# Kernel tuning notes

Hardware: AMD Instinct MI355X
Metric: run time of the kernel (lower is better)

The kernel has to match this reference:

```python
import jax, jax.numpy as jnp
import numpy as np

B, T, HID = 1, 2048, 2048
H = 16            # num_heads == num_key_value_heads
D = HID // H      # head_dim == feature_dim == 128
EPS = 1e-5


def _layer_norm(x, eps=1e-5):
    mu = jnp.mean(x, axis=-1, keepdims=True)
    var = jnp.mean((x - mu) ** 2, axis=-1, keepdims=True)
    return (x - mu) * jax.lax.rsqrt(var + eps)


def _feature_map(x, gamma, beta):
    # ReBased feature map, flatten=False (parallel mode): affine then LayerNorm
    return _layer_norm(x * gamma + beta)


def setup_inputs() -> dict:
    key = jax.random.key(0)
    ks = jax.random.split(key, 8)
    s = HID ** -0.5
    return {
        "hidden_states": jax.random.normal(ks[0], (B, T, HID), jnp.float32),
        "Wq": jax.random.normal(ks[1], (HID, HID), jnp.float32) * s,
        "Wk": jax.random.normal(ks[2], (HID, HID), jnp.float32) * s,
        "Wv": jax.random.normal(ks[3], (HID, HID), jnp.float32) * s,
        "Wo": jax.random.normal(ks[4], (HID, HID), jnp.float32) * s,
        "gamma": 1.0 + 0.1 * jax.random.normal(ks[5], (D,), jnp.float32),
        "beta": 0.1 * jax.random.normal(ks[6], (D,), jnp.float32),
    }


def reference(hidden_states, Wq, Wk, Wv, Wo, gamma, beta):
    b, t, _ = hidden_states.shape
    # projections (nn.Linear: x @ W.T), split into heads: [b, t, h, d]
    q = (hidden_states @ Wq.T).reshape(b, t, H, D)
    k = (hidden_states @ Wk.T).reshape(b, t, H, D)
    v = (hidden_states @ Wv.T).reshape(b, t, H, D)
    # ReBased feature map (no quadratic flatten in parallel mode)
    q = _feature_map(q, gamma, beta)
    k = _feature_map(k, gamma, beta)
    # parallel_rebased: scale q, quadratic score, causal mask, normalize
    q = q * (D ** -0.5)
    attn = jnp.einsum('bqhd,bkhd->bhqk', q, k) ** 2  # (q.k)^2
    mask = jnp.tril(jnp.ones((t, t), dtype=bool))
    attn = jnp.where(mask, attn, 0.0)
    o = jnp.einsum('bhqk,bkhd->bqhd', attn, v)       # [b, t, h, d]
    z = jnp.sum(attn, axis=-1)                       # [b, h, t]
    o = o / (jnp.swapaxes(z, 1, 2)[..., None] + EPS)
    o = o.reshape(b, t, H * D)
    return o @ Wo.T
```

## Files before the change

kernel.cpp:

```cpp
#include <hip/hip_runtime.h>
#include <hip/hip_bf16.h>
#include <stdint.h>

typedef __bf16 bf16;
typedef __bf16 v8bf __attribute__((ext_vector_type(8)));
typedef float  v4f  __attribute__((ext_vector_type(4)));

#define TSEQ   2048
#define HIDDIM 2048
#define NHEAD  16
#define HDIM   128

__device__ __forceinline__ void async16(void* lds, const void* g)
{
    __builtin_amdgcn_global_load_lds(
        (__attribute__((address_space(1))) void*)(uintptr_t)g,
        (__attribute__((address_space(3))) void*)(unsigned int)(uintptr_t)lds,
        16, 0, 0);
}

__global__ __launch_bounds__(256) void conv5(const float* __restrict__ s0, bf16* __restrict__ d0,
                                             const float* __restrict__ s1, bf16* __restrict__ d1,
                                             const float* __restrict__ s2, bf16* __restrict__ d2,
                                             const float* __restrict__ s3, bf16* __restrict__ d3,
                                             const float* __restrict__ s4, bf16* __restrict__ d4)
{
    const float* src; bf16* dst;
    switch (blockIdx.y) {
        case 0: src = s0; dst = d0; break;
        case 1: src = s1; dst = d1; break;
        case 2: src = s2; dst = d2; break;
        case 3: src = s3; dst = d3; break;
        default: src = s4; dst = d4; break;
    }
    const size_t i = ((size_t)blockIdx.x * 256 + threadIdx.x) * 8;
    const float4 a = *(const float4*)(src + i);
    const float4 b = *(const float4*)(src + i + 4);
    v8bf o;
    o[0] = (bf16)a.x; o[1] = (bf16)a.y; o[2] = (bf16)a.z; o[3] = (bf16)a.w;
    o[4] = (bf16)b.x; o[5] = (bf16)b.y; o[6] = (bf16)b.z; o[7] = (bf16)b.w;
    *(v8bf*)(dst + i) = o;
}


#define PBAR() do { __builtin_amdgcn_sched_barrier(0); __builtin_amdgcn_s_barrier(); \
                    __builtin_amdgcn_sched_barrier(0); } while (0)

#define ST(shalf, ghalf) do { \
    async16((shalf) + w*512,        (ghalf) + (size_t)(srow0)*2048); \
    async16((shalf) + 4096 + w*512, (ghalf) + (size_t)(srow0 + 64)*2048); \
} while (0)

#define RD_A(buf, mh) do { _Pragma("unroll") \
    for (int mi_ = 0; mi_ < 4; ++mi_) { \
        const bf16* p_ = &sA[(buf)*16384 + (wm*128 + (mh)*64 + mi_*16 + lr)*64]; \
        a[mi_][0] = *(const v8bf*)(p_ + c0); \
        a[mi_][1] = *(const v8bf*)(p_ + c1); } } while (0)

#define RD_B(buf, nh) do { _Pragma("unroll") \
    for (int nj_ = 0; nj_ < 2; ++nj_) { \
        const bf16* p_ = &sB[(buf)*16384 + (wn*64 + (nh)*32 + nj_*16 + lr)*64]; \
        b[(nh)*2+nj_][0] = *(const v8bf*)(p_ + c0); \
        b[(nh)*2+nj_][1] = *(const v8bf*)(p_ + c1); } } while (0)

#define MQ(mh, nh) do { _Pragma("unroll") \
    for (int mi_ = 0; mi_ < 4; ++mi_) { _Pragma("unroll") \
        for (int nj_ = 0; nj_ < 2; ++nj_) { \
            acc[(mh)*4+mi_][(nh)*2+nj_] = __builtin_amdgcn_mfma_f32_16x16x32_bf16( \
                a[mi_][0], b[(nh)*2+nj_][0], acc[(mh)*4+mi_][(nh)*2+nj_], 0, 0, 0); \
            acc[(mh)*4+mi_][(nh)*2+nj_] = __builtin_amdgcn_mfma_f32_16x16x32_bf16( \
                a[mi_][1], b[(nh)*2+nj_][1], acc[(mh)*4+mi_][(nh)*2+nj_], 0, 0, 0); \
        } } } while (0)

__global__ __launch_bounds__(512, 2) void gemm_qkv8(const bf16* __restrict__ A,
    const bf16* __restrict__ Wq, const bf16* __restrict__ Wk, const bf16* __restrict__ Wv,
    bf16* __restrict__ qb, bf16* __restrict__ kb, bf16* __restrict__ vb)
{
    __shared__ __attribute__((aligned(16))) bf16 sA[2*16384];
    __shared__ __attribute__((aligned(16))) bf16 sB[2*16384];
    const int which = blockIdx.x >> 3;
    const int n0 = (blockIdx.x & 7) * 256;
    const int m0 = blockIdx.y * 256;
    const bf16* B = (which == 0) ? Wq : (which == 1) ? Wk : Wv;
    bf16* C = (which == 0) ? qb : (which == 1) ? kb : vb;

    const int tid  = threadIdx.x, l = tid & 63, w = tid >> 6;
    const int wm   = w >> 2, wn = w & 3;
    const int quad = l >> 4, lr = l & 15;
    const int srow0 = w*8 + (l>>3);
    const int scol  = ((l & 7) ^ ((l >> 3) & 7)) * 8;
    const int c0 = (( quad     ) ^ (lr & 7)) * 8;
    const int c1 = ((quad + 4  ) ^ (lr & 7)) * 8;

    const bf16* Ag = A + (size_t)m0 * 2048 + scol;
    const bf16* Bg = B + (size_t)n0 * 2048 + scol;

    v4f  acc[8][4] = {};
    v8bf a[4][2], b[4][2];

    ST(&sA[0],          Ag);
    ST(&sA[8192],       Ag + (size_t)128*2048);
    ST(&sB[0],          Bg);
    ST(&sB[8192],       Bg + (size_t)128*2048);
    ST(&sB[16384],      Bg + 64);
    ST(&sB[16384+8192], Bg + (size_t)128*2048 + 64);
    asm volatile("s_waitcnt vmcnt(4)" ::: "memory");
    __builtin_amdgcn_s_barrier();
    __builtin_amdgcn_sched_barrier(0);

#pragma unroll 1
    for (int it = 0; it < 16; ++it) {
        const int k1 = it*128 + 64;
        const int k2 = (it*128 + 128) & 2047;
        const int k3 = (it*128 + 192) & 2047;

        RD_A(0, 0); RD_B(0, 0);
        ST(&sA[16384], Ag + k1);
        PBAR(); __builtin_amdgcn_s_setprio(1); MQ(0, 0); __builtin_amdgcn_s_setprio(0); PBAR();
        RD_B(0, 1);
        ST(&sA[16384+8192], Ag + (size_t)128*2048 + k1);
        PBAR(); __builtin_amdgcn_s_setprio(1); MQ(0, 1); __builtin_amdgcn_s_setprio(0); PBAR();
        RD_A(0, 1);
        ST(&sB[0], Bg + k2);
        PBAR(); __builtin_amdgcn_s_setprio(1); MQ(1, 0); __builtin_amdgcn_s_setprio(0); PBAR();
        ST(&sB[8192], Bg + (size_t)128*2048 + k2);
        asm volatile("s_waitcnt vmcnt(4)" ::: "memory");
        PBAR(); __builtin_amdgcn_s_setprio(1); MQ(1, 1); __builtin_amdgcn_s_setprio(0); PBAR();
        RD_A(1, 0); RD_B(1, 0);
        ST(&sA[0], Ag + k2);
        PBAR(); __builtin_amdgcn_s_setprio(1); MQ(0, 0); __builtin_amdgcn_s_setprio(0); PBAR();
        RD_B(1, 1);
        ST(&sA[8192], Ag + (size_t)128*2048 + k2);
        PBAR(); __builtin_amdgcn_s_setprio(1); MQ(0, 1); __builtin_amdgcn_s_setprio(0); PBAR();
        RD_A(1, 1);
        ST(&sB[16384], Bg + k3);
        PBAR(); __builtin_amdgcn_s_setprio(1); MQ(1, 0); __builtin_amdgcn_s_setprio(0); PBAR();
        ST(&sB[16384+8192], Bg + (size_t)128*2048 + k3);
        asm volatile("s_waitcnt vmcnt(4)" ::: "memory");
        PBAR(); __builtin_amdgcn_s_setprio(1); MQ(1, 1); __builtin_amdgcn_s_setprio(0); PBAR();
    }

#pragma unroll
    for (int mi = 0; mi < 8; ++mi) {
        const int row = m0 + wm*128 + (mi >> 2)*64 + (mi & 3)*16 + quad*4;
#pragma unroll
        for (int nj = 0; nj < 4; ++nj) {
            const int col = n0 + wn*64 + (nj >> 1)*32 + (nj & 1)*16 + lr;
#pragma unroll
            for (int r = 0; r < 4; ++r)
                C[(size_t)(row + r)*2048 + col] = (bf16)acc[mi][nj][r];
        }
    }
}

__global__ __launch_bounds__(256) void gemm_out(const bf16* __restrict__ A,
    const bf16* __restrict__ B, float* __restrict__ C)
{
    __shared__ __attribute__((aligned(16))) bf16 sA[128*32];
    __shared__ __attribute__((aligned(16))) bf16 sB[64*32];
    const int m0 = blockIdx.y * 128, n0 = blockIdx.x * 64;
    const int K = HIDDIM, ldc = HIDDIM;
    const int tid  = threadIdx.x;
    const int lane = tid & 63;
    const int w    = tid >> 6;
    const int wm   = w >> 1, wn = w & 1;
    const int quad = lane >> 4, lr = lane & 15;
    const int srow = lane >> 2;
    const int scol = (lane & 3) * 8;

    const bf16* gA0 = A + (size_t)(m0 + w*32 + srow) * K + scol;
    const bf16* gB0 = B + (size_t)(n0 + w*16 + srow) * K + scol;
    bf16* lA0 = &sA[w*1024];
    bf16* lB0 = &sB[w*512];

    v4f acc[4][2] = {};

    for (int kt = 0; kt < K; kt += 32) {
        __syncthreads();
        async16(lA0,       gA0 + kt);
        async16(lA0 + 512, gA0 + (size_t)16*K + kt);
        async16(lB0,       gB0 + kt);
        __syncthreads();
        v8bf a[4], b[2];
#pragma unroll
        for (int i = 0; i < 4; ++i)
            a[i] = *(const v8bf*)&sA[(wm*64 + i*16 + lr)*32 + quad*8];
#pragma unroll
        for (int j = 0; j < 2; ++j)
            b[j] = *(const v8bf*)&sB[(wn*32 + j*16 + lr)*32 + quad*8];
#pragma unroll
        for (int i = 0; i < 4; ++i)
#pragma unroll
            for (int j = 0; j < 2; ++j)
                acc[i][j] = __builtin_amdgcn_mfma_f32_16x16x32_bf16(a[i], b[j], acc[i][j], 0, 0, 0);
    }

#pragma unroll
    for (int i = 0; i < 4; ++i) {
        const int row_b = m0 + wm*64 + i*16 + quad*4;
#pragma unroll
        for (int j = 0; j < 2; ++j) {
            const int col = n0 + wn*32 + j*16 + lr;
#pragma unroll
            for (int r = 0; r < 4; ++r)
                C[(size_t)(row_b + r)*ldc + col] = acc[i][j][r];
        }
    }
}

__global__ __launch_bounds__(256) void fmap(bf16* __restrict__ qb, bf16* __restrict__ kb,
                                            const float* __restrict__ gamma,
                                            const float* __restrict__ beta)
{
    const int rid  = blockIdx.x * 4 + (threadIdx.x >> 6);
    const int lane = threadIdx.x & 63;
    bf16* base = (rid < TSEQ*NHEAD) ? (qb + (size_t)rid * HDIM)
                                    : (kb + (size_t)(rid - TSEQ*NHEAD) * HDIM);
    const float scale = (rid < TSEQ*NHEAD) ? 0.08838834764831845f : 1.0f;

    const bf16 x0b = base[lane*2], x1b = base[lane*2+1];
    const float g0 = gamma[lane*2], g1 = gamma[lane*2+1];
    const float b0 = beta[lane*2],  b1 = beta[lane*2+1];
    float x0 = (float)x0b*g0 + b0;
    float x1 = (float)x1b*g1 + b1;
    float s  = x0 + x1;
    float sq = x0*x0 + x1*x1;
#pragma unroll
    for (int off = 1; off < 64; off <<= 1) { s += __shfl_xor(s, off); sq += __shfl_xor(sq, off); }
    const float mu   = s * (1.0f/128.0f);
    float var        = sq * (1.0f/128.0f) - mu*mu;
    var = fmaxf(var, 0.0f);
    const float rstd = rsqrtf(var + 1e-5f);
    base[lane*2]   = (bf16)((x0 - mu) * rstd * scale);
    base[lane*2+1] = (bf16)((x1 - mu) * rstd * scale);
}

__global__ __launch_bounds__(256) void transpose2048(const bf16* __restrict__ src,
                                                     bf16* __restrict__ dst)
{
    __shared__ __attribute__((aligned(16))) bf16 tile[64][72];
    const int t0 = blockIdx.y * 64, c0 = blockIdx.x * 64;
    const int tid = threadIdx.x;
    const int r = tid >> 3;
    const int c = (tid & 7) * 8;
#pragma unroll
    for (int p = 0; p < 2; ++p) {
        const int rr = r + p*32;
        *(v8bf*)&tile[rr][c] = *(const v8bf*)(src + (size_t)(t0+rr)*HIDDIM + c0 + c);
    }
    __syncthreads();
#pragma unroll
    for (int p = 0; p < 2; ++p) {
        const int orow = r + p*32;
        v8bf o;
#pragma unroll
        for (int i = 0; i < 8; ++i) o[i] = tile[c + i][orow];
        *(v8bf*)(dst + (size_t)(c0+orow)*HIDDIM + t0 + c) = o;
    }
}

__global__ __launch_bounds__(512, 2) void attn(const bf16* __restrict__ qb,
                                               const bf16* __restrict__ kb,
                                               const bf16* __restrict__ vt,
                                               bf16* __restrict__ ob)
{
    __shared__ __attribute__((aligned(16))) bf16 sK[2*64*136];
    __shared__ __attribute__((aligned(16))) bf16 sV[2*128*72];
    __shared__ __attribute__((aligned(16))) bf16 sS[2*64*72];
    __shared__ __attribute__((aligned(16))) float sO[64*129];
    __shared__ __attribute__((aligned(16))) float sZ[64*17];

    const int h    = blockIdx.y;
    const int pr   = blockIdx.x;
    const int tid  = threadIdx.x, lane = tid & 63;
    const int w    = tid >> 6;
    const int g    = w >> 2;
    const int ww   = w & 3;
    const int quad = lane >> 4, lr = lane & 15;
    const int rs   = tid >> 4;
    const int cs   = (tid & 15) * 8;

#pragma unroll
    for (int ti = 0; ti < 2; ++ti) {
        const int tile = ti ? pr : (31 - pr);
        const int nch  = tile + 1;

        v8bf qa[4];
        {
            const bf16* q0 = qb + (size_t)(tile*64 + ww*16 + lr)*HIDDIM + h*HDIM + quad*8;
#pragma unroll
            for (int ks = 0; ks < 4; ++ks)
                qa[ks] = *(const v8bf*)(q0 + ks*32);
        }

        v4f  o[8] = {};
        float z[4] = {0.f, 0.f, 0.f, 0.f};

        v8bf curK[4], curV[4], nxtK[4], nxtV[4];
#pragma unroll
        for (int p = 0; p < 4; ++p) {
            curK[p] = *(const v8bf*)(kb + (size_t)(rs + p*32)*HIDDIM + h*HDIM + cs);
            curV[p] = *(const v8bf*)(vt + (size_t)(h*HDIM + rs + p*32)*HIDDIM + cs);
        }

        for (int ich = 0; ich < nch; ich += 2) {
            __syncthreads();
#pragma unroll
            for (int p = 0; p < 4; ++p) {
                const int r = rs + p*32;
                *(v8bf*)&sK[(r>>6)*8704 + (r&63)*136 + cs] = curK[p];
            }
#pragma unroll
            for (int p = 0; p < 4; ++p)
                *(v8bf*)&sV[(cs>>6)*9216 + (rs + p*32)*72 + (cs & 63)] = curV[p];

            if (ich + 2 < nch) {
                const int s1 = (ich + 2) * 64;
#pragma unroll
                for (int p = 0; p < 4; ++p) {
                    nxtK[p] = *(const v8bf*)(kb + (size_t)(s1 + rs + p*32)*HIDDIM + h*HDIM + cs);
                    nxtV[p] = *(const v8bf*)(vt + (size_t)(h*HDIM + rs + p*32)*HIDDIM + s1 + cs);
                }
            }
            __syncthreads();

            const int ch = ich + g;
            if (ch < nch) {
                const bf16* sKg = &sK[g*8704];
                const bf16* sVg = &sV[g*9216];
                bf16*       sSg = &sS[g*4608];
                const bool  diag = (ch == tile);
                const int   s0   = ch * 64;

                v8bf kbf[4][4];
#pragma unroll
                for (int nj = 0; nj < 4; ++nj)
#pragma unroll
                    for (int ks = 0; ks < 4; ++ks)
                        kbf[nj][ks] = *(const v8bf*)&sKg[(nj*16 + lr)*136 + ks*32 + quad*8];
                const int row_l = ww*16 + quad*4;
                const int qg    = tile*64 + row_l;
#pragma unroll
                for (int nj = 0; nj < 4; ++nj) {
                    v4f s4 = {0.f, 0.f, 0.f, 0.f};
#pragma unroll
                    for (int ks = 0; ks < 4; ++ks)
                        s4 = __builtin_amdgcn_mfma_f32_16x16x32_bf16(qa[ks], kbf[nj][ks], s4, 0, 0, 0);
                    const int col = nj*16 + lr;
                    const int sg  = s0 + col;
#pragma unroll
                    for (int r = 0; r < 4; ++r) {
                        float val = s4[r] * s4[r];
                        if (diag && (sg > qg + r)) val = 0.0f;
                        const bf16 vb16 = (bf16)val;
                        z[r] += (float)vb16;
                        sSg[(row_l + r)*72 + col] = vb16;
                    }
                }

#pragma unroll
                for (int ks = 0; ks < 2; ++ks) {
                    const v8bf sa = *(const v8bf*)&sSg[(ww*16 + lr)*72 + ks*32 + quad*8];
#pragma unroll
                    for (int nd = 0; nd < 8; ++nd) {
                        const v8bf vbf = *(const v8bf*)&sVg[(nd*16 + lr)*72 + ks*32 + quad*8];
                        o[nd] = __builtin_amdgcn_mfma_f32_16x16x32_bf16(sa, vbf, o[nd], 0, 0, 0);
                    }
                }
            }

            if (ich + 2 < nch) {
#pragma unroll
                for (int p = 0; p < 4; ++p) { curK[p] = nxtK[p]; curV[p] = nxtV[p]; }
            }
        }

        const int row_l = ww*16 + quad*4;
        __syncthreads();
        if (g == 1) {
#pragma unroll
            for (int nd = 0; nd < 8; ++nd)
#pragma unroll
                for (int r = 0; r < 4; ++r)
                    sO[(row_l + r)*129 + nd*16 + lr] = o[nd][r];
#pragma unroll
            for (int r = 0; r < 4; ++r)
                sZ[(row_l + r)*17 + lr] = z[r];
        }
        __syncthreads();
        if (g == 0) {
#pragma unroll
            for (int nd = 0; nd < 8; ++nd)
#pragma unroll
                for (int r = 0; r < 4; ++r)
                    o[nd][r] += sO[(row_l + r)*129 + nd*16 + lr];
#pragma unroll
            for (int r = 0; r < 4; ++r) {
                float zz = z[r] + sZ[(row_l + r)*17 + lr];
                zz += __shfl_xor(zz, 1); zz += __shfl_xor(zz, 2);
                zz += __shfl_xor(zz, 4); zz += __shfl_xor(zz, 8);
                z[r] = zz + 1e-5f;
            }
            const size_t rbase = (size_t)(tile*64 + row_l)*HIDDIM + h*HDIM;
#pragma unroll
            for (int nd = 0; nd < 8; ++nd) {
                const int col = nd*16 + lr;
#pragma unroll
                for (int r = 0; r < 4; ++r)
                    ob[rbase + (size_t)r*HIDDIM + col] = (bf16)(o[nd][r] / z[r]);
            }
        }
    }
}

extern "C" void kernel_launch(void* const* d_in, const int* in_sizes, int n_in,
                              void* d_out, int out_size, void* d_ws, size_t ws_size,
                              hipStream_t stream)
{
    const float* hs    = (const float*)d_in[0];
    const float* Wq    = (const float*)d_in[1];
    const float* Wk    = (const float*)d_in[2];
    const float* Wv    = (const float*)d_in[3];
    const float* Wo    = (const float*)d_in[4];
    const float* gamma = (const float*)d_in[5];
    const float* beta  = (const float*)d_in[6];
    float* outp = (float*)d_out;

    const size_t MAT = (size_t)TSEQ * HIDDIM;

    bf16* ws   = (bf16*)d_ws;
    bf16* hs_b = ws + 0*MAT;
    bf16* vt   = hs_b;
    bf16* Wv_b = ws + 1*MAT;
    bf16* Wo_b = ws + 2*MAT;
    bf16* qb   = ws + 3*MAT;
    bf16* kb   = ws + 4*MAT;
    bf16* vb   = ws + 5*MAT;
    bf16* ob   = vb;
    bf16* Wq_b = (bf16*)d_out;
    bf16* Wk_b = (bf16*)d_out + MAT;

    conv5<<<dim3(2048, 5), 256, 0, stream>>>(hs, hs_b, Wq, Wq_b, Wk, Wk_b, Wv, Wv_b, Wo, Wo_b);
    gemm_qkv8<<<dim3(24, 8), 512, 0, stream>>>(hs_b, Wq_b, Wk_b, Wv_b, qb, kb, vb);
    fmap<<<dim3(2*TSEQ*NHEAD/4), 256, 0, stream>>>(qb, kb, gamma, beta);
    transpose2048<<<dim3(32, 32), 256, 0, stream>>>(vb, vt);
    attn<<<dim3(16, 16), 512, 0, stream>>>(qb, kb, vt, ob);
    gemm_out<<<dim3(32, 16), 256, 0, stream>>>(ob, Wo_b, outp);
}
```

Baseline: 278.2 us.

## Retile QKV GEMM to 256x192 over concatenated weights to fill all CUs

The QKV projection now treats Wq, Wk and Wv as one contiguous 6144-row weight matrix and uses 256x192 tiles. That gives 256 workgroups instead of 192, so every CU on the device gets work. Workspace buffers are rearranged so the three converted weights sit back to back, and q/k move into the output buffer as scratch. The double-buffered LDS pipeline is reorganized for the narrower B tile. The epilogue now chooses the destination buffer per 16-column block. The smaller N-tile lowers reuse per workgroup and changes how load latency is hidden.

```diff
diff --git a/kernel.cpp b/kernel.cpp
--- a/kernel.cpp
+++ b/kernel.cpp
@@ -46,109 +46,98 @@
 #define PBAR() do { __builtin_amdgcn_sched_barrier(0); __builtin_amdgcn_s_barrier(); \
                     __builtin_amdgcn_sched_barrier(0); } while (0)
 
-#define ST(shalf, ghalf) do { \
-    async16((shalf) + w*512,        (ghalf) + (size_t)(srow0)*2048); \
-    async16((shalf) + 4096 + w*512, (ghalf) + (size_t)(srow0 + 64)*2048); \
-} while (0)
-
-#define RD_A(buf, mh) do { _Pragma("unroll") \
+#define STA(buf, ka) do { _Pragma("unroll") \
+    for (int s_ = 0; s_ < 4; ++s_) \
+        async16(&sA[(buf)*16384 + s_*4096 + w*512], \
+                Ag + (ka) + (size_t)(s_*64 + w*8 + (l>>3))*2048); } while (0)
+#define STB(buf, ka) do { _Pragma("unroll") \
+    for (int s_ = 0; s_ < 3; ++s_) \
+        async16(&sB[(buf)*12288 + s_*4096 + w*512], \
+                Bg + (ka) + (size_t)(s_*64 + w*8 + (l>>3))*2048); } while (0)
+
+#define RDA(buf, mh) do { _Pragma("unroll") \
     for (int mi_ = 0; mi_ < 4; ++mi_) { \
         const bf16* p_ = &sA[(buf)*16384 + (wm*128 + (mh)*64 + mi_*16 + lr)*64]; \
         a[mi_][0] = *(const v8bf*)(p_ + c0); \
         a[mi_][1] = *(const v8bf*)(p_ + c1); } } while (0)
-
-#define RD_B(buf, nh) do { _Pragma("unroll") \
-    for (int nj_ = 0; nj_ < 2; ++nj_) { \
-        const bf16* p_ = &sB[(buf)*16384 + (wn*64 + (nh)*32 + nj_*16 + lr)*64]; \
-        b[(nh)*2+nj_][0] = *(const v8bf*)(p_ + c0); \
-        b[(nh)*2+nj_][1] = *(const v8bf*)(p_ + c1); } } while (0)
-
-#define MQ(mh, nh) do { _Pragma("unroll") \
+#define RDB(buf) do { _Pragma("unroll") \
+    for (int nj_ = 0; nj_ < 3; ++nj_) { \
+        const bf16* p_ = &sB[(buf)*12288 + (wn*48 + nj_*16 + lr)*64]; \
+        b[nj_][0] = *(const v8bf*)(p_ + c0); \
+        b[nj_][1] = *(const v8bf*)(p_ + c1); } } while (0)
+
+#define MQ24(mh) do { _Pragma("unroll") \
     for (int mi_ = 0; mi_ < 4; ++mi_) { _Pragma("unroll") \
-        for (int nj_ = 0; nj_ < 2; ++nj_) { \
-            acc[(mh)*4+mi_][(nh)*2+nj_] = __builtin_amdgcn_mfma_f32_16x16x32_bf16( \
-                a[mi_][0], b[(nh)*2+nj_][0], acc[(mh)*4+mi_][(nh)*2+nj_], 0, 0, 0); \
-            acc[(mh)*4+mi_][(nh)*2+nj_] = __builtin_amdgcn_mfma_f32_16x16x32_bf16( \
-                a[mi_][1], b[(nh)*2+nj_][1], acc[(mh)*4+mi_][(nh)*2+nj_], 0, 0, 0); \
+        for (int nj_ = 0; nj_ < 3; ++nj_) { \
+            acc[(mh)*4+mi_][nj_] = __builtin_amdgcn_mfma_f32_16x16x32_bf16( \
+                a[mi_][0], b[nj_][0], acc[(mh)*4+mi_][nj_], 0, 0, 0); \
+            acc[(mh)*4+mi_][nj_] = __builtin_amdgcn_mfma_f32_16x16x32_bf16( \
+                a[mi_][1], b[nj_][1], acc[(mh)*4+mi_][nj_], 0, 0, 0); \
         } } } while (0)
 
-__global__ __launch_bounds__(512, 2) void gemm_qkv8(const bf16* __restrict__ A,
-    const bf16* __restrict__ Wq, const bf16* __restrict__ Wk, const bf16* __restrict__ Wv,
-    bf16* __restrict__ qb, bf16* __restrict__ kb, bf16* __restrict__ vb)
+__global__ __launch_bounds__(512, 2) void gemm_qkv192(const bf16* __restrict__ A,
+    const bf16* __restrict__ Wcat, bf16* __restrict__ qb, bf16* __restrict__ kb,
+    bf16* __restrict__ vb)
 {
     __shared__ __attribute__((aligned(16))) bf16 sA[2*16384];
-    __shared__ __attribute__((aligned(16))) bf16 sB[2*16384];
-    const int which = blockIdx.x >> 3;
-    const int n0 = (blockIdx.x & 7) * 256;
-    const int m0 = blockIdx.y * 256;
-    const bf16* B = (which == 0) ? Wq : (which == 1) ? Wk : Wv;
-    bf16* C = (which == 0) ? qb : (which == 1) ? kb : vb;
-
-    const int tid  = threadIdx.x, l = tid & 63, w = tid >> 6;
-    const int wm   = w >> 2, wn = w & 3;
+    __shared__ __attribute__((aligned(16))) bf16 sB[2*12288];
+    const int n0g = blockIdx.x * 192;
+    const int m0  = blockIdx.y * 256;
+
+    const int tid = threadIdx.x, l = tid & 63, w = tid >> 6;
+    const int wm = w >> 2, wn = w & 3;
     const int quad = l >> 4, lr = l & 15;
-    const int srow0 = w*8 + (l>>3);
-    const int scol  = ((l & 7) ^ ((l >> 3) & 7)) * 8;
-    const int c0 = (( quad     ) ^ (lr & 7)) * 8;
-    const int c1 = ((quad + 4  ) ^ (lr & 7)) * 8;
-
-    const bf16* Ag = A + (size_t)m0 * 2048 + scol;
-    const bf16* Bg = B + (size_t)n0 * 2048 + scol;
-
-    v4f  acc[8][4] = {};
-    v8bf a[4][2], b[4][2];
-
-    ST(&sA[0],          Ag);
-    ST(&sA[8192],       Ag + (size_t)128*2048);
-    ST(&sB[0],          Bg);
-    ST(&sB[8192],       Bg + (size_t)128*2048);
-    ST(&sB[16384],      Bg + 64);
-    ST(&sB[16384+8192], Bg + (size_t)128*2048 + 64);
-    asm volatile("s_waitcnt vmcnt(4)" ::: "memory");
+    const int scol = ((l & 7) ^ ((l >> 3) & 7)) * 8;
+    const int c0 = ((quad    ) ^ (lr & 7)) * 8;
+    const int c1 = ((quad + 4) ^ (lr & 7)) * 8;
+
+    const bf16* Ag = A    + (size_t)m0  * 2048 + scol;
+    const bf16* Bg = Wcat + (size_t)n0g * 2048 + scol;
+
+    v4f  acc[8][3] = {};
+    v8bf a[4][2], b[3][2];
+
+    STA(0, 0); STB(0, 0);
+    STB(1, 64); STA(1, 64);
+    asm volatile("s_waitcnt vmcnt(7)" ::: "memory");
     __builtin_amdgcn_s_barrier();
     __builtin_amdgcn_sched_barrier(0);
 
 #pragma unroll 1
     for (int it = 0; it < 16; ++it) {
-        const int k1 = it*128 + 64;
         const int k2 = (it*128 + 128) & 2047;
         const int k3 = (it*128 + 192) & 2047;
 
-        RD_A(0, 0); RD_B(0, 0);
-        ST(&sA[16384], Ag + k1);
-        PBAR(); __builtin_amdgcn_s_setprio(1); MQ(0, 0); __builtin_amdgcn_s_setprio(0); PBAR();
-        RD_B(0, 1);
-        ST(&sA[16384+8192], Ag + (size_t)128*2048 + k1);
-        PBAR(); __builtin_amdgcn_s_setprio(1); MQ(0, 1); __builtin_amdgcn_s_setprio(0); PBAR();
-        RD_A(0, 1);
-        ST(&sB[0], Bg + k2);
-        PBAR(); __builtin_amdgcn_s_setprio(1); MQ(1, 0); __builtin_amdgcn_s_setprio(0); PBAR();
-        ST(&sB[8192], Bg + (size_t)128*2048 + k2);
-        asm volatile("s_waitcnt vmcnt(4)" ::: "memory");
-        PBAR(); __builtin_amdgcn_s_setprio(1); MQ(1, 1); __builtin_amdgcn_s_setprio(0); PBAR();
-        RD_A(1, 0); RD_B(1, 0);
-        ST(&sA[0], Ag + k2);
-        PBAR(); __builtin_amdgcn_s_setprio(1); MQ(0, 0); __builtin_amdgcn_s_setprio(0); PBAR();
-        RD_B(1, 1);
-        ST(&sA[8192], Ag + (size_t)128*2048 + k2);
-        PBAR(); __builtin_amdgcn_s_setprio(1); MQ(0, 1); __builtin_amdgcn_s_setprio(0); PBAR();
-        RD_A(1, 1);
-        ST(&sB[16384], Bg + k3);
-        PBAR(); __builtin_amdgcn_s_setprio(1); MQ(1, 0); __builtin_amdgcn_s_setprio(0); PBAR();
-        ST(&sB[16384+8192], Bg + (size_t)128*2048 + k3);
-        asm volatile("s_waitcnt vmcnt(4)" ::: "memory");
-        PBAR(); __builtin_amdgcn_s_setprio(1); MQ(1, 1); __builtin_amdgcn_s_setprio(0); PBAR();
-    }
+        RDB(0); RDA(0, 0);
+        PBAR(); __builtin_amdgcn_s_setprio(1); MQ24(0); __builtin_amdgcn_s_setprio(0); PBAR();
+        RDA(0, 1);
+        STB(0, k2);
+        PBAR(); __builtin_amdgcn_s_setprio(1); MQ24(1); __builtin_amdgcn_s_setprio(0);
+        asm volatile("s_waitcnt vmcnt(3)" ::: "memory");
+        PBAR();
+        RDB(1); RDA(1, 0);
+        STA(0, k2);
+        PBAR(); __builtin_amdgcn_s_setprio(1); MQ24(0); __builtin_amdgcn_s_setprio(0); PBAR();
+        RDA(1, 1);
+        STB(1, k3); STA(1, k3);
+        PBAR(); __builtin_amdgcn_s_setprio(1); MQ24(1); __builtin_amdgcn_s_setprio(0);
+        asm volatile("s_waitcnt vmcnt(7)" ::: "memory");
+        PBAR();
+    }
+    asm volatile("s_waitcnt vmcnt(0)" ::: "memory");
 
 #pragma unroll
     for (int mi = 0; mi < 8; ++mi) {
         const int row = m0 + wm*128 + (mi >> 2)*64 + (mi & 3)*16 + quad*4;
 #pragma unroll
-        for (int nj = 0; nj < 4; ++nj) {
-            const int col = n0 + wn*64 + (nj >> 1)*32 + (nj & 1)*16 + lr;
+        for (int nj = 0; nj < 3; ++nj) {
+            const int colg  = n0g + wn*48 + nj*16;
+            const int which = colg >> 11;
+            bf16* Cb = (which == 0) ? qb : (which == 1) ? kb : vb;
+            const int lcol = (colg & 2047) + lr;
 #pragma unroll
             for (int r = 0; r < 4; ++r)
-                C[(size_t)(row + r)*2048 + col] = (bf16)acc[mi][nj][r];
+                Cb[(size_t)(row + r)*2048 + lcol] = (bf16)acc[mi][nj][r];
         }
     }
 }
@@ -431,17 +420,17 @@
     bf16* ws   = (bf16*)d_ws;
     bf16* hs_b = ws + 0*MAT;
     bf16* vt   = hs_b;
-    bf16* Wv_b = ws + 1*MAT;
-    bf16* Wo_b = ws + 2*MAT;
-    bf16* qb   = ws + 3*MAT;
-    bf16* kb   = ws + 4*MAT;
+    bf16* Wq_b = ws + 1*MAT;
+    bf16* Wk_b = ws + 2*MAT;
+    bf16* Wv_b = ws + 3*MAT;
+    bf16* Wo_b = ws + 4*MAT;
     bf16* vb   = ws + 5*MAT;
     bf16* ob   = vb;
-    bf16* Wq_b = (bf16*)d_out;
-    bf16* Wk_b = (bf16*)d_out + MAT;
+    bf16* qb   = (bf16*)d_out;
+    bf16* kb   = (bf16*)d_out + MAT;
 
     conv5<<<dim3(2048, 5), 256, 0, stream>>>(hs, hs_b, Wq, Wq_b, Wk, Wk_b, Wv, Wv_b, Wo, Wo_b);
-    gemm_qkv8<<<dim3(24, 8), 512, 0, stream>>>(hs_b, Wq_b, Wk_b, Wv_b, qb, kb, vb);
+    gemm_qkv192<<<dim3(32, 8), 512, 0, stream>>>(hs_b, Wq_b, qb, kb, vb);
     fmap<<<dim3(2*TSEQ*NHEAD/4), 256, 0, stream>>>(qb, kb, gamma, beta);
     transpose2048<<<dim3(32, 32), 256, 0, stream>>>(vb, vt);
     attn<<<dim3(16, 16), 512, 0, stream>>>(qb, kb, vt, ob);
```

Result: no change. 272.9 us (-1.9%).
